# Optimization experiments

Hardware: AMD Instinct MI355X
Metric: run time of the kernel (lower is better)

The kernel has to match this reference:

```python
import jax, jax.numpy as jnp
import numpy as np

# Multi-scale feature pyramid (H, W) per level: strides 8/16/32/64 on a ~512px image
SHAPES = ((64, 64), (32, 32), (16, 16), (8, 8))
N_HEADS, N_LEVELS, N_POINTS = 8, 4, 4
D_MODEL = 256
HEAD_DIM = D_MODEL // N_HEADS


def setup_inputs() -> dict:
    key = jax.random.key(0)
    ks = jax.random.split(key, 11)
    B, C = 4, D_MODEL
    Lv = sum(h * w for h, w in SHAPES)  # 5440
    Lq = Lv  # encoder self-attention: queries are the flattened features
    scale = 0.02
    return {
        "query": jax.random.normal(ks[0], (B, Lq, C), jnp.float32),
        "reference_points": jax.random.uniform(ks[1], (B, Lq, N_LEVELS, 2), jnp.float32),
        "value": jax.random.normal(ks[2], (B, Lv, C), jnp.float32),
        "W_off": jax.random.normal(ks[3], (C, N_HEADS * N_LEVELS * N_POINTS * 2), jnp.float32) * scale,
        "b_off": jax.random.normal(ks[4], (N_HEADS * N_LEVELS * N_POINTS * 2,), jnp.float32) * 0.5,
        "W_attn": jax.random.normal(ks[5], (C, N_HEADS * N_LEVELS * N_POINTS), jnp.float32) * scale,
        "b_attn": jax.random.normal(ks[6], (N_HEADS * N_LEVELS * N_POINTS,), jnp.float32) * scale,
        "W_val": jax.random.normal(ks[7], (C, C), jnp.float32) * scale,
        "b_val": jax.random.normal(ks[8], (C,), jnp.float32) * scale,
        "W_out": jax.random.normal(ks[9], (C, C), jnp.float32) * scale,
        "b_out": jax.random.normal(ks[10], (C,), jnp.float32) * scale,
    }


def _bilinear_sample(val, grid, H, W):
    """Replicates F.grid_sample(mode='bilinear', padding_mode='zeros', align_corners=False).

    val:  [N, C, H, W]
    grid: [N, Lq, P, 2] in [-1, 1] (x, y order)
    returns: [N, C, Lq, P]
    """
    N, C = val.shape[0], val.shape[1]
    # unnormalize (align_corners=False)
    x = (grid[..., 0] + 1.0) * 0.5 * W - 0.5  # [N, Lq, P]
    y = (grid[..., 1] + 1.0) * 0.5 * H - 0.5
    x0 = jnp.floor(x)
    y0 = jnp.floor(y)
    wx = x - x0  # fractional parts
    wy = y - y0
    flat = val.reshape(N, C, H * W)

    def gather(xi, yi):
        valid = (xi >= 0) & (xi < W) & (yi >= 0) & (yi < H)
        xc = jnp.clip(xi, 0, W - 1).astype(jnp.int32)
        yc = jnp.clip(yi, 0, H - 1).astype(jnp.int32)
        idx = yc * W + xc  # [N, Lq, P]
        g = jax.vmap(lambda v, i: v[:, i])(flat, idx)  # [N, C, Lq, P]
        return g * valid[:, None, :, :].astype(val.dtype)

    out = (gather(x0, y0) * ((1 - wx) * (1 - wy))[:, None]
           + gather(x0 + 1, y0) * (wx * (1 - wy))[:, None]
           + gather(x0, y0 + 1) * ((1 - wx) * wy)[:, None]
           + gather(x0 + 1, y0 + 1) * (wx * wy)[:, None])
    return out


def _ms_deform_attn(query, reference_points, value, W_off, b_off, W_attn, b_attn,
                    W_val, b_val, W_out, b_out):
    B, Lq, C = query.shape
    val = value @ W_val + b_val  # [B, Lv, C]
    val = val.reshape(B, -1, N_HEADS, HEAD_DIM)

    offsets = (query @ W_off + b_off).reshape(B, Lq, N_HEADS, N_LEVELS, N_POINTS, 2)
    weights = jax.nn.softmax(
        (query @ W_attn + b_attn).reshape(B, Lq, N_HEADS, N_LEVELS * N_POINTS), axis=-1
    ).reshape(B, Lq, N_HEADS, N_LEVELS, N_POINTS)

    # offset normalizer: (W, H) per level
    offset_norm = jnp.array([[w, h] for h, w in SHAPES], jnp.float32)
    # ref_dim == 2 branch
    locs = reference_points[:, :, None, :, None, :] + offsets / offset_norm[None, None, None, :, None, :]
    grids = 2.0 * locs - 1.0  # [B, Lq, nh, nl, np, 2]

    acc = jnp.zeros((B * N_HEADS, HEAD_DIM, Lq), query.dtype)
    start = 0
    for lid, (H, W) in enumerate(SHAPES):
        # [B, HW, nh, hd] -> [B*nh, hd, H, W]
        v = val[:, start:start + H * W].transpose(0, 2, 3, 1).reshape(B * N_HEADS, HEAD_DIM, H, W)
        g = grids[:, :, :, lid].transpose(0, 2, 1, 3, 4).reshape(B * N_HEADS, Lq, N_POINTS, 2)
        s = _bilinear_sample(v, g, H, W)  # [B*nh, hd, Lq, np]
        w = weights[:, :, :, lid].transpose(0, 2, 1, 3).reshape(B * N_HEADS, 1, Lq, N_POINTS)
        acc = acc + (s * w).sum(-1)
        start += H * W

    out = acc.reshape(B, D_MODEL, Lq).transpose(0, 2, 1)  # [B, Lq, C]
    return out @ W_out + b_out


def reference(query, reference_points, value, W_off, b_off, W_attn, b_attn,
              W_val, b_val, W_out, b_out):
    return _ms_deform_attn(query, reference_points, value, W_off, b_off,
                           W_attn, b_attn, W_val, b_val, W_out, b_out)
```

## Files before the change

### kernel.cpp

```cpp
#include <hip/hip_runtime.h>


typedef __attribute__((ext_vector_type(8))) _Float16 half8;
typedef __attribute__((ext_vector_type(4))) float f32x4;

typedef __attribute__((address_space(3))) unsigned int lds_uint;
typedef const __attribute__((address_space(1))) unsigned int g_uint;

__device__ __forceinline__ void load_lds16(const _Float16* g, _Float16* l) {
    __builtin_amdgcn_global_load_lds((g_uint*)g, (lds_uint*)l, 16, 0, 0);
}

__device__ __forceinline__ half8 splat8(_Float16 v) {
    half8 r = {v, v, v, v, v, v, v, v};
    return r;
}

#define M_TOTAL 21760

__global__ __launch_bounds__(256) void prep_weights(
    const float* __restrict__ W_val, const float* __restrict__ W_off,
    const float* __restrict__ W_attn, const float* __restrict__ W_out,
    const float* __restrict__ b_off, const float* __restrict__ b_attn,
    _Float16* __restrict__ wt_val, _Float16* __restrict__ wt_qcat,
    _Float16* __restrict__ wt_out, float* __restrict__ bcat)
{
    const int r = blockIdx.x;
    const int k = threadIdx.x;
    if (r < 256) {
        wt_val[r * 256 + k] = (_Float16)W_val[k * 256 + r];
    } else if (r < 640) {
        const int n = r - 256;
        const float v = (n < 256) ? W_off[k * 256 + n] : W_attn[k * 128 + (n - 256)];
        wt_qcat[n * 256 + k] = (_Float16)v;
    } else if (r < 896) {
        const int n = r - 640;
        wt_out[n * 256 + k] = (_Float16)W_out[k * 256 + n];
    } else {
        bcat[k] = b_off[k];
        if (k < 128) bcat[256 + k] = b_attn[k];
    }
}

__global__ __launch_bounds__(256) void cvt_f32_f16(
    const float* __restrict__ value, const float* __restrict__ query,
    _Float16* __restrict__ val16, _Float16* __restrict__ q16)
{
    const size_t per = (size_t)M_TOTAL * 256 / 8;
    size_t idx = (size_t)blockIdx.x * 256 + threadIdx.x;
    const float* src;
    _Float16* dst;
    if (idx < per) { src = value; dst = val16; }
    else { src = query; dst = q16; idx -= per; }
    const float4 lo = *(const float4*)(src + idx * 8);
    const float4 hi = *(const float4*)(src + idx * 8 + 4);
    half8 o = {(_Float16)lo.x, (_Float16)lo.y, (_Float16)lo.z, (_Float16)lo.w,
               (_Float16)hi.x, (_Float16)hi.y, (_Float16)hi.z, (_Float16)hi.w};
    *(half8*)(dst + idx * 8) = o;
}

__global__ __launch_bounds__(256) void gemm_f16(
    const _Float16* __restrict__ A, const _Float16* __restrict__ Bt,
    const float* __restrict__ bias, void* __restrict__ Cv,
    int NN, int outf16)
{
    __shared__ _Float16 Ah[128 * 32];
    __shared__ _Float16 Bh[128 * 32];

    const int tid = threadIdx.x;
    const int bm = blockIdx.y * 128;
    const int bn = blockIdx.x * 128;
    const int wave = tid >> 6, lane = tid & 63;
    const int wm = (wave & 1) * 64, wn = (wave >> 1) * 64;
    const int ml = lane & 15, kq = (lane >> 4) * 8;
    const int lr = lane >> 2;
    const int lk = (lane & 3) * 8;

    const f32x4 zero4 = {0.f, 0.f, 0.f, 0.f};
    f32x4 acc[4][4];
#pragma unroll
    for (int i = 0; i < 4; ++i)
#pragma unroll
        for (int j = 0; j < 4; ++j) acc[i][j] = zero4;

    for (int kt = 0; kt < 8; ++kt) {
        const int k0 = kt * 32;
        __syncthreads();
#pragma unroll
        for (int t = 0; t < 2; ++t) {
            const int row = wave * 32 + t * 16;
            load_lds16(A + (size_t)(bm + row + lr) * 256 + k0 + lk,
                       Ah + (size_t)row * 32);
            load_lds16(Bt + (size_t)(bn + row + lr) * 256 + k0 + lk,
                       Bh + (size_t)row * 32);
        }
        __syncthreads();

        half8 af[4], bf[4];
#pragma unroll
        for (int i = 0; i < 4; ++i)
            af[i] = *(const half8*)(Ah + (wm + i * 16 + ml) * 32 + kq);
#pragma unroll
        for (int j = 0; j < 4; ++j)
            bf[j] = *(const half8*)(Bh + (wn + j * 16 + ml) * 32 + kq);
#pragma unroll
        for (int i = 0; i < 4; ++i)
#pragma unroll
            for (int j = 0; j < 4; ++j)
                acc[i][j] = __builtin_amdgcn_mfma_f32_16x16x32_f16(af[i], bf[j], acc[i][j], 0, 0, 0);
    }

    const int r0 = (lane >> 4) * 4;
#pragma unroll
    for (int j = 0; j < 4; ++j) {
        const int col = bn + wn + j * 16 + ml;
        const float bj = bias[col];
#pragma unroll
        for (int i = 0; i < 4; ++i) {
            const size_t rbase = (size_t)(bm + wm + i * 16 + r0) * NN + col;
#pragma unroll
            for (int r = 0; r < 4; ++r) {
                const float v = acc[i][j][r] + bj;
                if (outf16)
                    ((_Float16*)Cv)[rbase + (size_t)r * NN] = (_Float16)v;
                else
                    ((float*)Cv)[rbase + (size_t)r * NN] = v;
            }
        }
    }
}

__global__ __launch_bounds__(256) void sample_f16(
    const _Float16* __restrict__ valh,
    const float* __restrict__ refp,
    const _Float16* __restrict__ offh,
    _Float16* __restrict__ acc_out)
{
    const int wave = threadIdx.x >> 6, lane = threadIdx.x & 63;
    const int q2 = lane >> 5, sl = lane & 31;
    const int bq = blockIdx.x * 8 + wave * 2 + q2;
    const int b = bq / 5440;
    const int h = sl >> 2;
    const int d8 = (sl & 3) * 8;

    const _Float16* off_row = offh + (size_t)bq * 384 + h * 32;
    const _Float16* att_row = offh + (size_t)bq * 384 + 256 + h * 16;
    const float* rp = refp + (size_t)bq * 8;

    float offv[32];
#pragma unroll
    for (int i = 0; i < 4; ++i) {
        const half8 t = *(const half8*)(off_row + i * 8);
#pragma unroll
        for (int j = 0; j < 8; ++j) offv[i * 8 + j] = (float)t[j];
    }
    float lg[16];
    {
        const half8 t0 = *(const half8*)(att_row);
        const half8 t1 = *(const half8*)(att_row + 8);
#pragma unroll
        for (int j = 0; j < 8; ++j) { lg[j] = (float)t0[j]; lg[8 + j] = (float)t1[j]; }
    }
    float mx = -1e30f;
#pragma unroll
    for (int i = 0; i < 16; ++i) mx = fmaxf(mx, lg[i]);
    float s = 0.f;
#pragma unroll
    for (int i = 0; i < 16; ++i) { lg[i] = __expf(lg[i] - mx); s += lg[i]; }
    const float inv = 1.f / s;

    const float4 rp01 = *(const float4*)rp;
    const float4 rp23 = *(const float4*)(rp + 4);
    const float rxs[4] = {rp01.x, rp01.z, rp23.x, rp23.z};
    const float rys[4] = {rp01.y, rp01.w, rp23.y, rp23.w};

    const int Ws_[4] = {64, 32, 16, 8};
    const int starts_[4] = {0, 4096, 5120, 5376};

    half8 acc = splat8((_Float16)0.f);
#pragma unroll
    for (int l = 0; l < 4; ++l) {
        const int W = Ws_[l];
        const float fW = (float)W;
        const _Float16* vbase = valh + ((size_t)(b * 5440 + starts_[l])) * 256 + h * 32 + d8;
        const float rx = rxs[l], ry = rys[l];
#pragma unroll
        for (int p = 0; p < 4; ++p) {
            const int pi = l * 4 + p;
            const float aw = lg[pi] * inv;
            const float x = fmaf(rx, fW, offv[pi * 2 + 0]) - 0.5f;
            const float y = fmaf(ry, fW, offv[pi * 2 + 1]) - 0.5f;
            const float x0f = floorf(x), y0f = floorf(y);
            const int x0 = (int)x0f, y0 = (int)y0f;
            const float wx = x - x0f, wy = y - y0f;
            const bool okx0 = ((unsigned)x0 < (unsigned)W);
            const bool okx1 = ((unsigned)(x0 + 1) < (unsigned)W);
            const bool oky0 = ((unsigned)y0 < (unsigned)W);
            const bool oky1 = ((unsigned)(y0 + 1) < (unsigned)W);
            const int xc0 = min(max(x0, 0), W - 1);
            const int xc1 = min(max(x0 + 1, 0), W - 1);
            const int yc0 = min(max(y0, 0), W - 1);
            const int yc1 = min(max(y0 + 1, 0), W - 1);
            const float w00 = (okx0 & oky0) ? (1.f - wx) * (1.f - wy) * aw : 0.f;
            const float w10 = (okx1 & oky0) ? wx * (1.f - wy) * aw : 0.f;
            const float w01 = (okx0 & oky1) ? (1.f - wx) * wy * aw : 0.f;
            const float w11 = (okx1 & oky1) ? wx * wy * aw : 0.f;

            const half8 c00 = *(const half8*)(vbase + (size_t)(yc0 * W + xc0) * 256);
            const half8 c10 = *(const half8*)(vbase + (size_t)(yc0 * W + xc1) * 256);
            const half8 c01 = *(const half8*)(vbase + (size_t)(yc1 * W + xc0) * 256);
            const half8 c11 = *(const half8*)(vbase + (size_t)(yc1 * W + xc1) * 256);

            acc += c00 * splat8((_Float16)w00);
            acc += c10 * splat8((_Float16)w10);
            acc += c01 * splat8((_Float16)w01);
            acc += c11 * splat8((_Float16)w11);
        }
    }

    *(half8*)(acc_out + (size_t)bq * 256 + h * 32 + d8) = acc;
}

extern "C" void kernel_launch(void* const* d_in, const int* in_sizes, int n_in,
                              void* d_out, int out_size, void* d_ws, size_t ws_size,
                              hipStream_t stream) {
    const float* query  = (const float*)d_in[0];
    const float* refp   = (const float*)d_in[1];
    const float* value  = (const float*)d_in[2];
    const float* W_off  = (const float*)d_in[3];
    const float* b_off  = (const float*)d_in[4];
    const float* W_attn = (const float*)d_in[5];
    const float* b_attn = (const float*)d_in[6];
    const float* W_val  = (const float*)d_in[7];
    const float* b_val  = (const float*)d_in[8];
    const float* W_out  = (const float*)d_in[9];
    const float* b_out  = (const float*)d_in[10];
    float* out = (float*)d_out;

    const size_t M = M_TOTAL;

    _Float16* val16 = (_Float16*)d_ws;
    _Float16* q16   = val16 + M * 256;
    _Float16* valh  = q16 + M * 256;
    _Float16* offh  = valh + M * 256;
    _Float16* wtv   = offh + M * 384;
    _Float16* wtq   = wtv + 256 * 256;
    _Float16* wto   = wtq + 384 * 256;
    float* bcat     = (float*)(wto + 256 * 256);
    _Float16* acc16 = val16;

    dim3 blk(256);
    prep_weights<<<dim3(897), blk, 0, stream>>>(W_val, W_off, W_attn, W_out,
                                                b_off, b_attn, wtv, wtq, wto, bcat);
    cvt_f32_f16<<<dim3(2 * M * 256 / 8 / 256), blk, 0, stream>>>(value, query, val16, q16);
    gemm_f16<<<dim3(2, 170), blk, 0, stream>>>(val16, wtv, b_val, valh, 256, 1);
    gemm_f16<<<dim3(3, 170), blk, 0, stream>>>(q16, wtq, bcat, offh, 384, 1);
    sample_f16<<<dim3(M / 8), blk, 0, stream>>>(valh, refp, offh, acc16);
    gemm_f16<<<dim3(2, 170), blk, 0, stream>>>(acc16, wto, b_out, out, 256, 0);
}
```

Baseline: 185.1 us.

## Merge prep and convert kernels, fuse value/query GEMMs, shrink GEMM N-tile

Folds weight transposition and the f32-to-f16 conversion into one launch, and runs the value and offset/attention projections in a single grid. The output projection also moves to the new core. The GEMM N-tile drops from 128 to 64, which doubles the block count (340 to 680 per 256-wide GEMM) to fill more CUs on MI355X. The goal is fewer launches and better occupancy, at the cost of less B-tile reuse per block and more redundant A loads.

```diff
diff --git a/kernel.cpp b/kernel.cpp
--- a/kernel.cpp
+++ b/kernel.cpp
@@ -18,36 +18,35 @@
 
 #define M_TOTAL 21760
 
-__global__ __launch_bounds__(256) void prep_weights(
+__global__ __launch_bounds__(256) void prep_cvt(
     const float* __restrict__ W_val, const float* __restrict__ W_off,
     const float* __restrict__ W_attn, const float* __restrict__ W_out,
     const float* __restrict__ b_off, const float* __restrict__ b_attn,
+    const float* __restrict__ value, const float* __restrict__ query,
     _Float16* __restrict__ wt_val, _Float16* __restrict__ wt_qcat,
-    _Float16* __restrict__ wt_out, float* __restrict__ bcat)
+    _Float16* __restrict__ wt_out, float* __restrict__ bcat,
+    _Float16* __restrict__ val16, _Float16* __restrict__ q16)
 {
     const int r = blockIdx.x;
     const int k = threadIdx.x;
-    if (r < 256) {
-        wt_val[r * 256 + k] = (_Float16)W_val[k * 256 + r];
-    } else if (r < 640) {
-        const int n = r - 256;
-        const float v = (n < 256) ? W_off[k * 256 + n] : W_attn[k * 128 + (n - 256)];
-        wt_qcat[n * 256 + k] = (_Float16)v;
-    } else if (r < 896) {
-        const int n = r - 640;
-        wt_out[n * 256 + k] = (_Float16)W_out[k * 256 + n];
-    } else {
-        bcat[k] = b_off[k];
-        if (k < 128) bcat[256 + k] = b_attn[k];
-    }
-}
-
-__global__ __launch_bounds__(256) void cvt_f32_f16(
-    const float* __restrict__ value, const float* __restrict__ query,
-    _Float16* __restrict__ val16, _Float16* __restrict__ q16)
-{
+    if (r < 897) {
+        if (r < 256) {
+            wt_val[r * 256 + k] = (_Float16)W_val[k * 256 + r];
+        } else if (r < 640) {
+            const int n = r - 256;
+            const float v = (n < 256) ? W_off[k * 256 + n] : W_attn[k * 128 + (n - 256)];
+            wt_qcat[n * 256 + k] = (_Float16)v;
+        } else if (r < 896) {
+            const int n = r - 640;
+            wt_out[n * 256 + k] = (_Float16)W_out[k * 256 + n];
+        } else {
+            bcat[k] = b_off[k];
+            if (k < 128) bcat[256 + k] = b_attn[k];
+        }
+        return;
+    }
     const size_t per = (size_t)M_TOTAL * 256 / 8;
-    size_t idx = (size_t)blockIdx.x * 256 + threadIdx.x;
+    size_t idx = (size_t)(r - 897) * 256 + k;
     const float* src;
     _Float16* dst;
     if (idx < per) { src = value; dst = val16; }
@@ -59,29 +58,29 @@
     *(half8*)(dst + idx * 8) = o;
 }
 
-__global__ __launch_bounds__(256) void gemm_f16(
+__device__ __forceinline__ void gemm_core(
     const _Float16* __restrict__ A, const _Float16* __restrict__ Bt,
     const float* __restrict__ bias, void* __restrict__ Cv,
-    int NN, int outf16)
+    int NN, int outf16, int mt, int nt)
 {
     __shared__ _Float16 Ah[128 * 32];
-    __shared__ _Float16 Bh[128 * 32];
+    __shared__ _Float16 Bh[64 * 32];
 
     const int tid = threadIdx.x;
-    const int bm = blockIdx.y * 128;
-    const int bn = blockIdx.x * 128;
+    const int bm = mt * 128;
+    const int bn = nt * 64;
     const int wave = tid >> 6, lane = tid & 63;
-    const int wm = (wave & 1) * 64, wn = (wave >> 1) * 64;
+    const int wm = (wave & 1) * 64, wn = (wave >> 1) * 32;
     const int ml = lane & 15, kq = (lane >> 4) * 8;
     const int lr = lane >> 2;
     const int lk = (lane & 3) * 8;
 
     const f32x4 zero4 = {0.f, 0.f, 0.f, 0.f};
-    f32x4 acc[4][4];
+    f32x4 acc[4][2];
 #pragma unroll
     for (int i = 0; i < 4; ++i)
 #pragma unroll
-        for (int j = 0; j < 4; ++j) acc[i][j] = zero4;
+        for (int j = 0; j < 2; ++j) acc[i][j] = zero4;
 
     for (int kt = 0; kt < 8; ++kt) {
         const int k0 = kt * 32;
@@ -91,28 +90,31 @@
             const int row = wave * 32 + t * 16;
             load_lds16(A + (size_t)(bm + row + lr) * 256 + k0 + lk,
                        Ah + (size_t)row * 32);
+        }
+        {
+            const int row = wave * 16;
             load_lds16(Bt + (size_t)(bn + row + lr) * 256 + k0 + lk,
                        Bh + (size_t)row * 32);
         }
         __syncthreads();
 
-        half8 af[4], bf[4];
+        half8 af[4], bf[2];
 #pragma unroll
         for (int i = 0; i < 4; ++i)
             af[i] = *(const half8*)(Ah + (wm + i * 16 + ml) * 32 + kq);
 #pragma unroll
-        for (int j = 0; j < 4; ++j)
+        for (int j = 0; j < 2; ++j)
             bf[j] = *(const half8*)(Bh + (wn + j * 16 + ml) * 32 + kq);
 #pragma unroll
         for (int i = 0; i < 4; ++i)
 #pragma unroll
-            for (int j = 0; j < 4; ++j)
+            for (int j = 0; j < 2; ++j)
                 acc[i][j] = __builtin_amdgcn_mfma_f32_16x16x32_f16(af[i], bf[j], acc[i][j], 0, 0, 0);
     }
 
     const int r0 = (lane >> 4) * 4;
 #pragma unroll
-    for (int j = 0; j < 4; ++j) {
+    for (int j = 0; j < 2; ++j) {
         const int col = bn + wn + j * 16 + ml;
         const float bj = bias[col];
 #pragma unroll
@@ -128,6 +130,29 @@
             }
         }
     }
+}
+
+__global__ __launch_bounds__(256) void gemm12(
+    const _Float16* __restrict__ val16, const _Float16* __restrict__ q16,
+    const _Float16* __restrict__ wtv, const _Float16* __restrict__ wtq,
+    const float* __restrict__ b_val, const float* __restrict__ bcat,
+    _Float16* __restrict__ valh, _Float16* __restrict__ offh)
+{
+    int id = blockIdx.x;
+    if (id < 680) {
+        gemm_core(val16, wtv, b_val, valh, 256, 1, id >> 2, id & 3);
+    } else {
+        id -= 680;
+        gemm_core(q16, wtq, bcat, offh, 384, 1, id / 6, id % 6);
+    }
+}
+
+__global__ __launch_bounds__(256) void gemm_single(
+    const _Float16* __restrict__ A, const _Float16* __restrict__ Bt,
+    const float* __restrict__ bias, void* __restrict__ Cv, int NN, int outf16)
+{
+    const int id = blockIdx.x;
+    gemm_core(A, Bt, bias, Cv, NN, outf16, id >> 2, id & 3);
 }
 
 __global__ __launch_bounds__(256) void sample_f16(
@@ -250,11 +275,10 @@
     _Float16* acc16 = val16;
 
     dim3 blk(256);
-    prep_weights<<<dim3(897), blk, 0, stream>>>(W_val, W_off, W_attn, W_out,
-                                                b_off, b_attn, wtv, wtq, wto, bcat);
-    cvt_f32_f16<<<dim3(2 * M * 256 / 8 / 256), blk, 0, stream>>>(value, query, val16, q16);
-    gemm_f16<<<dim3(2, 170), blk, 0, stream>>>(val16, wtv, b_val, valh, 256, 1);
-    gemm_f16<<<dim3(3, 170), blk, 0, stream>>>(q16, wtq, bcat, offh, 384, 1);
+    prep_cvt<<<dim3(897 + 5440), blk, 0, stream>>>(
+        W_val, W_off, W_attn, W_out, b_off, b_attn, value, query,
+        wtv, wtq, wto, bcat, val16, q16);
+    gemm12<<<dim3(1700), blk, 0, stream>>>(val16, q16, wtv, wtq, b_val, bcat, valh, offh);
     sample_f16<<<dim3(M / 8), blk, 0, stream>>>(valh, refp, offh, acc16);
-    gemm_f16<<<dim3(2, 170), blk, 0, stream>>>(acc16, wto, b_out, out, 256, 0);
-}
+    gemm_single<<<dim3(680), blk, 0, stream>>>(acc16, wto, b_out, out, 256, 0);
+}
```

Result: no change. 186.2 us (+0.6%).
